# Performance work log

Hardware: AMD Instinct MI355X
Metric: run time of the kernel (lower is better)

The kernel has to match this reference:

```python
import jax, jax.numpy as jnp
import numpy as np

D_MODEL = 1024
NUM_HEADS = 16
D_K = D_MODEL // NUM_HEADS
ROPE_THETA = 10000.0


def apply_rope(x, pos):
    # x: [B, H, S, d_k], pos: [S] int
    half = x.shape[-1] // 2
    inv_freq = ROPE_THETA ** (-jnp.arange(half, dtype=jnp.float32) * 2.0 / x.shape[-1])
    ang = pos.astype(jnp.float32)[:, None] * inv_freq[None, :]  # [S, half]
    cos, sin = jnp.cos(ang), jnp.sin(ang)
    x1 = x[..., 0::2]
    x2 = x[..., 1::2]
    r1 = x1 * cos - x2 * sin
    r2 = x1 * sin + x2 * cos
    return jnp.stack([r1, r2], axis=-1).reshape(x.shape)


def setup_inputs() -> dict:
    key = jax.random.key(0)
    ks = jax.random.split(key, 5)
    B, S = 4, 2048
    scale = 1.0 / np.sqrt(D_MODEL)
    x = jax.random.normal(ks[0], (B, S, D_MODEL), dtype=jnp.float32)
    w_q = jax.random.normal(ks[1], (D_MODEL, D_MODEL), dtype=jnp.float32) * scale
    w_k = jax.random.normal(ks[2], (D_MODEL, D_MODEL), dtype=jnp.float32) * scale
    w_v = jax.random.normal(ks[3], (D_MODEL, D_MODEL), dtype=jnp.float32) * scale
    w_o = jax.random.normal(ks[4], (D_MODEL, D_MODEL), dtype=jnp.float32) * scale
    token_positions = jnp.arange(S, dtype=jnp.int32)
    return {"x": x, "w_q": w_q, "w_k": w_k, "w_v": w_v, "w_o": w_o, "token_positions": token_positions}


def reference(x, w_q, w_k, w_v, w_o, token_positions):
    B, S, _ = x.shape
    def proj(w):
        return (x @ w.T).reshape(B, S, NUM_HEADS, D_K).transpose(0, 2, 1, 3)  # [B,H,S,d_k]
    q, k, v = proj(w_q), proj(w_k), proj(w_v)
    q = apply_rope(q, token_positions)
    k = apply_rope(k, token_positions)
    logits = jnp.einsum('bhid,bhjd->bhij', q, k) / jnp.sqrt(jnp.float32(D_K))
    causal = jnp.tril(jnp.ones((S, S), dtype=bool))
    logits = jnp.where(causal[None, None], logits, -jnp.inf)
    weights = jax.nn.softmax(logits, axis=-1)
    attn = jnp.einsum('bhij,bhjd->bhid', weights, v)  # [B,H,S,d_k]
    attn = attn.transpose(0, 2, 1, 3).reshape(B, S, D_MODEL)
    return attn @ w_o.T
```

## Files before the change

### kernel.cpp

```cpp
#include <hip/hip_runtime.h>
#include <hip/hip_bf16.h>
#include <stdint.h>

#define DM   1024
#define SEQ  2048
#define BATCH 4
#define NH   16
#define DK   64
#define NTK  16

typedef __attribute__((ext_vector_type(8))) __bf16 bf16x8;
typedef __attribute__((ext_vector_type(4))) float f32x4;
typedef __attribute__((ext_vector_type(4))) unsigned short ushort4_t;

typedef __attribute__((address_space(1))) const unsigned int GU32;
typedef __attribute__((address_space(3))) unsigned int LU32;

__device__ inline void gl_lds16(const void* g, void* l) {
  __builtin_amdgcn_global_load_lds((GU32*)g, (LU32*)l, 16, 0, 0);
}

__device__ inline f32x4 mfma16(bf16x8 a, bf16x8 b, f32x4 c) {
  return __builtin_amdgcn_mfma_f32_16x16x32_bf16(a, b, c, 0, 0, 0);
}

__device__ inline unsigned short f2bf(float f) {
  unsigned u = __float_as_uint(f);
  u += 0x7fffu + ((u >> 16) & 1u);
  return (unsigned short)(u >> 16);
}

__device__ inline unsigned cvt_pk_bf16(float a, float b) {
  unsigned r;
  asm("v_cvt_pk_bf16_f32 %0, %1, %2" : "=v"(r) : "v"(a), "v"(b));
  return r;
}

__device__ inline int swz_of(int r) { return ((r & 6) << 2) | ((r & 1) << 5); }

__global__ void prep_kernel(const float* __restrict__ x,
                            const float* __restrict__ wq, const float* __restrict__ wk,
                            const float* __restrict__ wv, const float* __restrict__ wo,
                            const int* __restrict__ tp,
                            unsigned short* __restrict__ xbf,
                            unsigned short* __restrict__ wbf,
                            float2* __restrict__ tab)
{
  const int NX4 = (BATCH*SEQ*DM)/4;
  const int NW4 = (DM*DM)/4;
  int idx = blockIdx.x*256 + threadIdx.x;
  if (idx < NX4) {
    float4 v = ((const float4*)x)[idx];
    ushort4_t o; o[0]=f2bf(v.x); o[1]=f2bf(v.y); o[2]=f2bf(v.z); o[3]=f2bf(v.w);
    ((ushort4_t*)xbf)[idx] = o;
  } else if (idx < NX4 + 4*NW4) {
    int t = idx - NX4;
    int wsel = t >> 18;
    int off = t & (NW4-1);
    const float* src = (wsel==0) ? wq : (wsel==1) ? wk : (wsel==2) ? wv : wo;
    float4 v = ((const float4*)src)[off];
    ushort4_t o; o[0]=f2bf(v.x); o[1]=f2bf(v.y); o[2]=f2bf(v.z); o[3]=f2bf(v.w);
    ((ushort4_t*)wbf)[wsel*NW4 + off] = o;
  } else {
    int t = idx - NX4 - 4*NW4;
    if (t < SEQ*32) {
      int s = t >> 5, i = t & 31;
      float invf = exp2f(-(float)i * (13.287712379549449f/32.0f));
      float ang = (float)tp[s] * invf;
      float sn, cs; sincosf(ang, &sn, &cs);
      tab[t] = make_float2(cs, sn);
    }
  }
}

template<int MODE>
__global__ __launch_bounds__(256, 2)
void gemm_db(const unsigned short* __restrict__ A,
             const unsigned short* __restrict__ Wall,
             unsigned short* __restrict__ qbf,
             unsigned short* __restrict__ kbf,
             unsigned short* __restrict__ vt,
             float* __restrict__ ofp,
             const float2* __restrict__ tab)
{
  __shared__ __align__(16) char lds[65536];
  const int tid = threadIdx.x;
  const int bid = blockIdx.x;
  int sel, mt, nt;
  if (MODE == 0) {
    sel = bid >> 9;
    int r = bid & 511;
    int xcd = r & 7, idx = r >> 3;
    mt = xcd*8 + (idx >> 3);  nt = idx & 7;
  } else {
    sel = 3;
    int xcd = bid & 7, idx = bid >> 3;
    mt = xcd*8 + (idx >> 3);  nt = idx & 7;
  }
  const unsigned short* Bm = Wall + (size_t)sel*DM*DM;
  const int a0 = mt*128, b0r = nt*128;
  const int w = tid>>6, lane = tid&63, ln = lane&15, g = lane>>4;
  const int wm = (w>>1)*64, wn = (w&1)*64;

  const char* src[8];
  {
    int rr = tid >> 3;
    int c  = (tid & 7) * 8;
    #pragma unroll
    for (int i = 0; i < 4; ++i) {
      int r_ = i*32 + rr;
      int cs = c ^ swz_of(r_);
      src[i]   = (const char*)(A  + (size_t)(a0  + r_)*DM + cs);
      src[i+4] = (const char*)(Bm + (size_t)(b0r + r_)*DM + cs);
    }
  }

  int offA[4], offB[4];
  #pragma unroll
  for (int m = 0; m < 4; ++m) {
    int R  = wm + m*16 + ln;
    offA[m] = R*128 + ((g*8 ^ swz_of(R)) * 2);
    int Rb = wn + m*16 + ln;
    offB[m] = 16384 + Rb*128 + ((g*8 ^ swz_of(Rb)) * 2);
  }

  f32x4 acc[4][4];
  #pragma unroll
  for (int i=0;i<4;i++)
    #pragma unroll
    for (int j=0;j<4;j++) acc[i][j] = (f32x4){0.f,0.f,0.f,0.f};

  #pragma unroll
  for (int i = 0; i < 8; ++i) gl_lds16(src[i],       lds +         i*4096 + tid*16);
  #pragma unroll
  for (int i = 0; i < 8; ++i) gl_lds16(src[i] + 128, lds + 32768 + i*4096 + tid*16);

  for (int t = 0; t < NTK; ++t) {
    char* sb = lds + (t & 1) * 32768;
    if (t < NTK-1) asm volatile("s_waitcnt vmcnt(8)" ::: "memory");
    else           asm volatile("s_waitcnt vmcnt(0)" ::: "memory");
    __builtin_amdgcn_sched_barrier(0);
    __builtin_amdgcn_s_barrier();
    asm volatile("" ::: "memory");
    __builtin_amdgcn_sched_barrier(0);

    bf16x8 fa[4][2], fb[4][2];
    #pragma unroll
    for (int m = 0; m < 4; ++m) {
      fa[m][0] = *(const bf16x8*)(sb + offA[m]);
      fa[m][1] = *(const bf16x8*)(sb + (offA[m] ^ 64));
      fb[m][0] = *(const bf16x8*)(sb + offB[m]);
      fb[m][1] = *(const bf16x8*)(sb + (offB[m] ^ 64));
    }
    asm volatile("s_waitcnt lgkmcnt(0)" ::: "memory");
    __builtin_amdgcn_sched_barrier(0);
    __builtin_amdgcn_s_barrier();
    asm volatile("" ::: "memory");
    __builtin_amdgcn_sched_barrier(0);

    if (t + 2 < NTK) {
      const int kb = (t + 2) * 128;
      #pragma unroll
      for (int i = 0; i < 8; ++i)
        gl_lds16(src[i] + kb, sb + i*4096 + tid*16);
    }
    __builtin_amdgcn_s_setprio(1);
    #pragma unroll
    for (int h = 0; h < 2; ++h)
      #pragma unroll
      for (int m = 0; m < 4; ++m)
        #pragma unroll
        for (int n = 0; n < 4; ++n)
          acc[m][n] = mfma16(fa[m][h], fb[n][h], acc[m][n]);
    __builtin_amdgcn_s_setprio(0);
  }

  if (MODE == 1) {
    #pragma unroll
    for (int i=0;i<4;i++) {
      int m = a0 + wm + i*16 + g*4;
      #pragma unroll
      for (int jn=0;jn<4;jn++) {
        int n = b0r + wn + jn*16 + ln;
        #pragma unroll
        for (int j=0;j<4;j++)
          ofp[(size_t)(m+j)*DM + n] = acc[i][jn][j];
      }
    }
  } else if (sel == 2) {
    #pragma unroll
    for (int i=0;i<4;i++) {
      int m0 = a0 + wm + i*16 + g*4;
      int bb = m0>>11, s0 = m0&2047;
      #pragma unroll
      for (int jn=0;jn<4;jn++) {
        int n = b0r + wn + jn*16 + ln;
        int h = n>>6, d = n&63;
        ushort4_t o4;
        #pragma unroll
        for (int j=0;j<4;j++) o4[j] = f2bf(acc[i][jn][j]);
        *(ushort4_t*)&vt[(((size_t)bb*NH + h)*DK + d)*SEQ + s0] = o4;
      }
    }
  } else {
    unsigned short* dst = sel ? kbf : qbf;
    const float qs = sel ? 1.0f : 0.1803368802f;
    #pragma unroll
    for (int jn=0;jn<4;jn++) {
      int n = b0r + wn + jn*16 + ln;
      int h = n>>6, d = n&63, di = d>>1, par = d&1;
      #pragma unroll
      for (int i=0;i<4;i++) {
        #pragma unroll
        for (int j=0;j<4;j++) {
          int m = a0 + wm + i*16 + g*4 + j;
          int bb = m>>11, s = m&2047;
          float v = acc[i][jn][j];
          float pv = __shfl_xor(v, 1);
          float2 cssn = tab[s*32 + di];
          float r = par ? (v*cssn.x + pv*cssn.y) : (v*cssn.x - pv*cssn.y);
          dst[((size_t)(bb*NH + h)*SEQ + s)*DK + d] = f2bf(r*qs);
        }
      }
    }
  }
}

__global__ __launch_bounds__(256, 2)
void attn_fa(const unsigned short* __restrict__ qbf,
             const unsigned short* __restrict__ kbf,
             const unsigned short* __restrict__ vtg,
             unsigned short* __restrict__ attnbf)
{
  __shared__ unsigned short Kt[64][72];
  __shared__ unsigned short Vt[64][72];
  __shared__ unsigned short Pl[4][16][72];
  const int bh = blockIdx.x, qb = 31 - blockIdx.y;
  const int tid = threadIdx.x, w = tid>>6, lane = tid&63, ln = lane&15, g = lane>>4;
  const int q0 = qb*64 + w*16;

  const unsigned short* qrow = qbf + ((size_t)bh*SEQ + q0 + ln)*DK;
  bf16x8 qf0 = *(const bf16x8*)(qrow + g*8);
  bf16x8 qf1 = *(const bf16x8*)(qrow + 32 + g*8);

  f32x4 o[4];
  #pragma unroll
  for (int f=0;f<4;f++) o[f] = (f32x4){0.f,0.f,0.f,0.f};
  float m_run = -1e30f, l_run = 0.f;

  const int sr = tid>>2, sc16 = (tid&3)*16;
  const unsigned short* ksrc = kbf + ((size_t)bh*SEQ + sr)*DK + sc16;
  const unsigned short* vsrc = vtg + ((size_t)bh*DK + sr)*SEQ + sc16;
  const int qg = q0 + ln;

  for (int t = 0; t <= qb; ++t) {
    const int kv0 = t*64;
    __syncthreads();
    {
      bf16x8 k0v = *(const bf16x8*)(ksrc + (size_t)kv0*DK);
      bf16x8 k1v = *(const bf16x8*)(ksrc + (size_t)kv0*DK + 8);
      bf16x8 v0v = *(const bf16x8*)(vsrc + kv0);
      bf16x8 v1v = *(const bf16x8*)(vsrc + kv0 + 8);
      *(bf16x8*)&Kt[sr][sc16]   = k0v;
      *(bf16x8*)&Kt[sr][sc16+8] = k1v;
      *(bf16x8*)&Vt[sr][sc16]   = v0v;
      *(bf16x8*)&Vt[sr][sc16+8] = v1v;
    }
    __syncthreads();

    f32x4 sa[4];
    #pragma unroll
    for (int kvf=0;kvf<4;kvf++) {
      f32x4 z = (f32x4){0.f,0.f,0.f,0.f};
      bf16x8 kf0 = *(const bf16x8*)&Kt[kvf*16 + ln][g*8];
      bf16x8 kf1 = *(const bf16x8*)&Kt[kvf*16 + ln][32 + g*8];
      z = mfma16(kf0, qf0, z);
      z = mfma16(kf1, qf1, z);
      sa[kvf] = z;
    }

    float sc[4][4];
    float lmax = -1e30f;
    if (t == qb) {
      #pragma unroll
      for (int kvf=0;kvf<4;kvf++)
        #pragma unroll
        for (int j=0;j<4;j++) {
          int kv = kv0 + kvf*16 + g*4 + j;
          float v = (kv <= qg) ? sa[kvf][j] : -1e30f;
          sc[kvf][j] = v; lmax = fmaxf(lmax, v);
        }
    } else {
      #pragma unroll
      for (int kvf=0;kvf<4;kvf++)
        #pragma unroll
        for (int j=0;j<4;j++) {
          float v = sa[kvf][j];
          sc[kvf][j] = v; lmax = fmaxf(lmax, v);
        }
    }
    lmax = fmaxf(lmax, __shfl_xor(lmax, 16));
    lmax = fmaxf(lmax, __shfl_xor(lmax, 32));

    if (!__all(lmax - m_run <= 8.0f)) {
      float mnew = fmaxf(m_run, lmax);
      float corr = exp2f(m_run - mnew);
      l_run *= corr;
      #pragma unroll
      for (int j=0;j<4;j++) {
        float cj = __shfl(corr, g*4 + j);
        #pragma unroll
        for (int f=0;f<4;f++) o[f][j] *= cj;
      }
      m_run = mnew;
    }

    float lsum = 0.f;
    #pragma unroll
    for (int kvf=0;kvf<4;kvf++) {
      float p0 = exp2f(sc[kvf][0] - m_run);
      float p1 = exp2f(sc[kvf][1] - m_run);
      float p2 = exp2f(sc[kvf][2] - m_run);
      float p3 = exp2f(sc[kvf][3] - m_run);
      lsum += (p0+p1)+(p2+p3);
      uint2 pk;
      pk.x = cvt_pk_bf16(p0, p1);
      pk.y = cvt_pk_bf16(p2, p3);
      *(uint2*)&Pl[w][ln][kvf*16 + g*4] = pk;
    }
    lsum += __shfl_xor(lsum, 16);
    lsum += __shfl_xor(lsum, 32);
    l_run += lsum;

    asm volatile("s_waitcnt lgkmcnt(0)" ::: "memory");

    #pragma unroll
    for (int c=0;c<2;c++) {
      bf16x8 pf = *(const bf16x8*)&Pl[w][ln][c*32 + g*8];
      #pragma unroll
      for (int f=0;f<4;f++) {
        bf16x8 vf = *(const bf16x8*)&Vt[f*16 + ln][c*32 + g*8];
        o[f] = mfma16(pf, vf, o[f]);
      }
    }
  }

  const int bb = bh>>4, h = bh&15;
  #pragma unroll
  for (int j=0;j<4;j++) {
    float linv = 1.0f / __shfl(l_run, g*4 + j);
    int s = q0 + g*4 + j;
    #pragma unroll
    for (int f=0;f<4;f++)
      attnbf[((size_t)bb*SEQ + s)*DM + h*DK + f*16 + ln] = f2bf(o[f][j]*linv);
  }
}

extern "C" void kernel_launch(void* const* d_in, const int* in_sizes, int n_in,
                              void* d_out, int out_size, void* d_ws, size_t ws_size,
                              hipStream_t stream)
{
  const float* x  = (const float*)d_in[0];
  const float* wq = (const float*)d_in[1];
  const float* wk = (const float*)d_in[2];
  const float* wv = (const float*)d_in[3];
  const float* wo = (const float*)d_in[4];
  const int*   tp = (const int*)d_in[5];

  const size_t XB = (size_t)BATCH*SEQ*DM*2;
  const size_t WB = (size_t)DM*DM*2;

  char* ws = (char*)d_ws;
  unsigned short* xbf = (unsigned short*)(ws);
  unsigned short* qbf = (unsigned short*)(ws + XB);
  unsigned short* kbf = (unsigned short*)(ws + 2*XB);
  unsigned short* vt  = (unsigned short*)(ws + 3*XB);
  unsigned short* abf = (unsigned short*)(ws + 4*XB);
  unsigned short* wbf = (unsigned short*)(ws + 5*XB);
  float2* tab = (float2*)(ws + 5*XB + 4*WB);

  prep_kernel<<<12544, 256, 0, stream>>>(x, wq, wk, wv, wo, tp, xbf, wbf, tab);

  gemm_db<0><<<1536, 256, 0, stream>>>(xbf, wbf, qbf, kbf, vt, nullptr, tab);
  attn_fa<<<dim3(64,32), 256, 0, stream>>>(qbf, kbf, vt, abf);
  gemm_db<1><<<512, 256, 0, stream>>>(abf, wbf, nullptr, nullptr, nullptr,
                                      (float*)d_out, nullptr);
}
```

Measured before the change: 179.6 us.

## Load K/V fragments directly into registers with prefetch, drop shared staging

The attention kernel no longer stages K and V tiles through shared memory with two block barriers per iteration. Each wave now loads its MFMA fragments straight from global memory into registers and prefetches the next tile's K and V while the current tile is being processed. exp2f is also replaced by the raw v_exp_f32 instruction. The trade-offs are that every wave now fetches the full K/V tile redundantly (four times the global/L2 traffic) and register pressure rises, which may reduce occupancy.

```diff
diff --git a/kernel.cpp b/kernel.cpp
--- a/kernel.cpp
+++ b/kernel.cpp
@@ -33,6 +33,12 @@
 __device__ inline unsigned cvt_pk_bf16(float a, float b) {
   unsigned r;
   asm("v_cvt_pk_bf16_f32 %0, %1, %2" : "=v"(r) : "v"(a), "v"(b));
+  return r;
+}
+
+__device__ inline float fexp2(float x) {
+  float r;
+  asm("v_exp_f32 %0, %1" : "=v"(r) : "v"(x));
   return r;
 }
 
@@ -232,8 +238,6 @@
              const unsigned short* __restrict__ vtg,
              unsigned short* __restrict__ attnbf)
 {
-  __shared__ unsigned short Kt[64][72];
-  __shared__ unsigned short Vt[64][72];
   __shared__ unsigned short Pl[4][16][72];
   const int bh = blockIdx.x, qb = 31 - blockIdx.y;
   const int tid = threadIdx.x, w = tid>>6, lane = tid&63, ln = lane&15, g = lane>>4;
@@ -243,68 +247,65 @@
   bf16x8 qf0 = *(const bf16x8*)(qrow + g*8);
   bf16x8 qf1 = *(const bf16x8*)(qrow + 32 + g*8);
 
+  const unsigned short* kp = kbf + ((size_t)bh*SEQ + ln)*DK + g*8;
+  const unsigned short* vp = vtg + ((size_t)bh*DK + ln)*SEQ + g*8;
+
+  bf16x8 kf[4][2], vf[4][2];
+  #pragma unroll
+  for (int a=0;a<4;a++) {
+    kf[a][0] = *(const bf16x8*)(kp + a*16*DK);
+    kf[a][1] = *(const bf16x8*)(kp + a*16*DK + 32);
+    vf[a][0] = *(const bf16x8*)(vp + (size_t)a*16*SEQ);
+    vf[a][1] = *(const bf16x8*)(vp + (size_t)a*16*SEQ + 32);
+  }
+
   f32x4 o[4];
   #pragma unroll
   for (int f=0;f<4;f++) o[f] = (f32x4){0.f,0.f,0.f,0.f};
   float m_run = -1e30f, l_run = 0.f;
-
-  const int sr = tid>>2, sc16 = (tid&3)*16;
-  const unsigned short* ksrc = kbf + ((size_t)bh*SEQ + sr)*DK + sc16;
-  const unsigned short* vsrc = vtg + ((size_t)bh*DK + sr)*SEQ + sc16;
   const int qg = q0 + ln;
 
   for (int t = 0; t <= qb; ++t) {
-    const int kv0 = t*64;
-    __syncthreads();
-    {
-      bf16x8 k0v = *(const bf16x8*)(ksrc + (size_t)kv0*DK);
-      bf16x8 k1v = *(const bf16x8*)(ksrc + (size_t)kv0*DK + 8);
-      bf16x8 v0v = *(const bf16x8*)(vsrc + kv0);
-      bf16x8 v1v = *(const bf16x8*)(vsrc + kv0 + 8);
-      *(bf16x8*)&Kt[sr][sc16]   = k0v;
-      *(bf16x8*)&Kt[sr][sc16+8] = k1v;
-      *(bf16x8*)&Vt[sr][sc16]   = v0v;
-      *(bf16x8*)&Vt[sr][sc16+8] = v1v;
-    }
-    __syncthreads();
-
     f32x4 sa[4];
     #pragma unroll
     for (int kvf=0;kvf<4;kvf++) {
       f32x4 z = (f32x4){0.f,0.f,0.f,0.f};
-      bf16x8 kf0 = *(const bf16x8*)&Kt[kvf*16 + ln][g*8];
-      bf16x8 kf1 = *(const bf16x8*)&Kt[kvf*16 + ln][32 + g*8];
-      z = mfma16(kf0, qf0, z);
-      z = mfma16(kf1, qf1, z);
+      z = mfma16(kf[kvf][0], qf0, z);
+      z = mfma16(kf[kvf][1], qf1, z);
       sa[kvf] = z;
     }
-
-    float sc[4][4];
+    if (t < qb) {
+      const unsigned short* kn = kp + (size_t)(t+1)*64*DK;
+      #pragma unroll
+      for (int a=0;a<4;a++) {
+        kf[a][0] = *(const bf16x8*)(kn + a*16*DK);
+        kf[a][1] = *(const bf16x8*)(kn + a*16*DK + 32);
+      }
+    }
+
     float lmax = -1e30f;
     if (t == qb) {
+      const int kv0 = t*64;
       #pragma unroll
       for (int kvf=0;kvf<4;kvf++)
         #pragma unroll
         for (int j=0;j<4;j++) {
           int kv = kv0 + kvf*16 + g*4 + j;
           float v = (kv <= qg) ? sa[kvf][j] : -1e30f;
-          sc[kvf][j] = v; lmax = fmaxf(lmax, v);
+          sa[kvf][j] = v; lmax = fmaxf(lmax, v);
         }
     } else {
       #pragma unroll
       for (int kvf=0;kvf<4;kvf++)
         #pragma unroll
-        for (int j=0;j<4;j++) {
-          float v = sa[kvf][j];
-          sc[kvf][j] = v; lmax = fmaxf(lmax, v);
-        }
+        for (int j=0;j<4;j++) lmax = fmaxf(lmax, sa[kvf][j]);
     }
     lmax = fmaxf(lmax, __shfl_xor(lmax, 16));
     lmax = fmaxf(lmax, __shfl_xor(lmax, 32));
 
     if (!__all(lmax - m_run <= 8.0f)) {
       float mnew = fmaxf(m_run, lmax);
-      float corr = exp2f(m_run - mnew);
+      float corr = fexp2(m_run - mnew);
       l_run *= corr;
       #pragma unroll
       for (int j=0;j<4;j++) {
@@ -318,10 +319,10 @@
     float lsum = 0.f;
     #pragma unroll
     for (int kvf=0;kvf<4;kvf++) {
-      float p0 = exp2f(sc[kvf][0] - m_run);
-      float p1 = exp2f(sc[kvf][1] - m_run);
-      float p2 = exp2f(sc[kvf][2] - m_run);
-      float p3 = exp2f(sc[kvf][3] - m_run);
+      float p0 = fexp2(sa[kvf][0] - m_run);
+      float p1 = fexp2(sa[kvf][1] - m_run);
+      float p2 = fexp2(sa[kvf][2] - m_run);
+      float p3 = fexp2(sa[kvf][3] - m_run);
       lsum += (p0+p1)+(p2+p3);
       uint2 pk;
       pk.x = cvt_pk_bf16(p0, p1);
@@ -338,9 +339,15 @@
     for (int c=0;c<2;c++) {
       bf16x8 pf = *(const bf16x8*)&Pl[w][ln][c*32 + g*8];
       #pragma unroll
-      for (int f=0;f<4;f++) {
-        bf16x8 vf = *(const bf16x8*)&Vt[f*16 + ln][c*32 + g*8];
-        o[f] = mfma16(pf, vf, o[f]);
+      for (int f=0;f<4;f++)
+        o[f] = mfma16(pf, vf[f][c], o[f]);
+    }
+    if (t < qb) {
+      const unsigned short* vn = vp + (t+1)*64;
+      #pragma unroll
+      for (int a=0;a<4;a++) {
+        vf[a][0] = *(const bf16x8*)(vn + (size_t)a*16*SEQ);
+        vf[a][1] = *(const bf16x8*)(vn + (size_t)a*16*SEQ + 32);
       }
     }
   }
```

New measurement: 340.2 us. +89.4%, slower.
